# Optimization experiments

Measured on AMD Instinct MI355X. Metric: run time of the kernel, lower is better.

Reference implementation:

```python
import jax, jax.numpy as jnp
import numpy as np

# init config (from init_kwargs)
NUM_ANCHORS = 5
NUM_CLASSES = 80
ANCHORS = jnp.array([[0.57273, 0.677385], [1.87446, 2.06253], [3.33843, 5.47434],
                     [7.88282, 3.52778], [9.77052, 9.16828]], dtype=jnp.float32)
MAX_BOXES = 50  # hard-coded loop bound in build_targets


def setup_inputs() -> dict:
    key = jax.random.key(0)
    k1, k2 = jax.random.split(key)
    output = jax.random.normal(k1, (64, 425, 38, 38), dtype=jnp.float32)
    # target: (nB, 50*5) of [cls, cx, cy, w, h] normalized to (0,1); strictly
    # positive entries -> all 50 boxes valid (original loop breaks at first 0).
    target = jax.random.uniform(k2, (64, 250), dtype=jnp.float32, minval=0.02, maxval=0.98)
    return {"output": output, "target": target, "reqd_class_index": 14}


def _cls_mask(target, nH, nW):
    """Vectorized build_targets: only cls_mask affects the returned loss.
    For each valid GT box, best anchor = argmax IoU of (0,0,aw,ah) vs (0,0,gw,gh)
    (first max wins, matching the strict > in the Python loop); mark cell
    (b, best_n, gj, gi)."""
    nB = target.shape[0]
    tgt = target.reshape(nB, MAX_BOXES, 5)
    # loop breaks at first t with target[b][5t+1]==0 -> cumulative validity
    valid = jnp.cumprod((tgt[:, :, 1] != 0).astype(jnp.int32), axis=1) > 0
    gx = tgt[:, :, 1] * nW
    gy = tgt[:, :, 2] * nH
    gw = tgt[:, :, 3] * nW  # (nB, T)
    gh = tgt[:, :, 4] * nH
    gi = jnp.clip(jnp.floor(gx).astype(jnp.int32), 0, nW - 1)
    gj = jnp.clip(jnp.floor(gy).astype(jnp.int32), 0, nH - 1)
    aw, ah = ANCHORS[:, 0], ANCHORS[:, 1]  # (nA,)
    # centered-box IoU: intersection widths are min of the widths
    inter = jnp.minimum(gw[..., None], aw) * jnp.minimum(gh[..., None], ah)  # (nB,T,nA)
    iou = inter / (gw[..., None] * gh[..., None] + aw * ah - inter)
    best_n = jnp.argmax(iou, axis=-1).astype(jnp.int32)  # (nB, T), first-max tiebreak
    b = jnp.arange(nB, dtype=jnp.int32)[:, None]
    flat = ((b * NUM_ANCHORS + best_n) * nH + gj) * nW + gi  # (nB, T)
    n_cells = nB * NUM_ANCHORS * nH * nW
    mask = jnp.zeros((n_cells,), jnp.int32).at[flat.ravel()].max(valid.ravel().astype(jnp.int32))
    return mask > 0


def reference(output, target, reqd_class_index):
    nB, _, nH, nW = output.shape
    out = output.reshape(nB, NUM_ANCHORS, 5 + NUM_CLASSES, nH, nW)
    # class logits -> (nB, nA, nH, nW, nC), matching torch's
    # view(nB*nA, nC, nH*nW).transpose(1,2).view(-1, nC) flattening order
    cls_logits = jnp.transpose(out[:, :, 5:, :, :], (0, 1, 3, 4, 2))
    probs = jax.nn.softmax(cls_logits, axis=-1)
    p = probs[..., reqd_class_index].reshape(-1)  # prob of required class per cell
    mask = _cls_mask(target, nH, nW)
    m = mask.astype(p.dtype)
    # L1Loss(cls_prob2, 0, size_average=True) over selected cells == masked mean
    loss = jnp.sum(p * m) / jnp.sum(m)
    max_class_prob = jnp.max(jnp.where(mask, p, -jnp.inf))
    return loss, max_class_prob
```

## Files before the change

kernel.cpp:

```cpp
#include <hip/hip_runtime.h>
#include <stdint.h>
#include <math.h>

#define NUM_ANCHORS 5
#define NUM_CLASSES 80
#define MAX_BOXES   50


__global__ void __launch_bounds__(64)
build_list(const float* __restrict__ target,
           int* __restrict__ cnt,
           int* __restrict__ list,
           int nH, int nW) {
#pragma clang fp contract(off)
    int b = blockIdx.x;
    int lane = threadIdx.x;
    const float* t = target + (long)b * MAX_BOXES * 5;
    float x = 1.0f, y = 0.0f, w = 0.0f, h = 0.0f;
    if (lane < MAX_BOXES) {
        x = t[lane * 5 + 1];
        y = t[lane * 5 + 2];
        w = t[lane * 5 + 3];
        h = t[lane * 5 + 4];
    }
    unsigned long long zb = __ballot(lane < MAX_BOXES && x == 0.0f);
    int first_zero = zb ? (__ffsll(zb) - 1) : MAX_BOXES;
    bool valid = lane < first_zero;

    float gx = x * (float)nW;
    float gy = y * (float)nH;
    float gw = w * (float)nW;
    float gh = h * (float)nH;
    int gi = min(max((int)floorf(gx), 0), nW - 1);
    int gj = min(max((int)floorf(gy), 0), nH - 1);

    const float aw[NUM_ANCHORS] = {0.57273f, 1.87446f, 3.33843f, 7.88282f, 9.77052f};
    const float ah[NUM_ANCHORS] = {0.677385f, 2.06253f, 5.47434f, 3.52778f, 9.16828f};
    int best = 0; float bestiou = -1.0f;
    #pragma unroll
    for (int n = 0; n < NUM_ANCHORS; ++n) {
        float inter = fminf(gw, aw[n]) * fminf(gh, ah[n]);
        float uni   = gw * gh + aw[n] * ah[n] - inter;
        float iou   = inter / uni;
        if (iou > bestiou) { bestiou = iou; best = n; }
    }
    int flat = ((b * NUM_ANCHORS + best) * nH + gj) * nW + gi;

    unsigned long long vmask = __ballot(valid);
    bool dup = false;
    for (int j = 0; j < MAX_BOXES; ++j) {
        int fj = __shfl(flat, j, 64);
        dup |= (j < lane) && (((vmask >> j) & 1ull) != 0) && (fj == flat);
    }
    bool keep = valid && !dup;
    unsigned long long kmask = __ballot(keep);
    if (keep) {
        int rank = __popcll(kmask & ((1ull << lane) - 1ull));
        list[b * MAX_BOXES + rank] = flat;
    }
    if (lane == 0) cnt[b] = (int)__popcll(kmask);
}

__global__ void __launch_bounds__(256)
reduce_list(const float* __restrict__ output,
            const int* __restrict__ cnt,
            const int* __restrict__ list,
            float* __restrict__ psum,
            float* __restrict__ pmax,
            const int* __restrict__ reqd,
            int HW, int total) {
    __shared__ float sp[4];
    __shared__ float sm[4];
    int lane = threadIdx.x & 63;
    int wave = threadIdx.x >> 6;
    int g = blockIdx.x * 4 + wave;
    float p = 0.0f, pm = -INFINITY;
    if (g < total) {
        int b    = g / MAX_BOXES;
        int slot = g - b * MAX_BOXES;
        if (slot < cnt[b]) {
            int cell = list[g];
            int ba = cell / HW;
            int hw = cell - ba * HW;
            const float* ptr = output + ((long)(ba * (5 + NUM_CLASSES) + 5)) * HW + hw;
            float v0 = ptr[(long)lane * HW];
            float v1 = (lane < NUM_CLASSES - 64) ? ptr[(long)(lane + 64) * HW] : -INFINITY;
            float mx = fmaxf(v0, v1);
            #pragma unroll
            for (int off = 32; off; off >>= 1) mx = fmaxf(mx, __shfl_xor(mx, off, 64));
            float e0 = expf(v0 - mx);
            float e1 = (lane < NUM_CLASSES - 64) ? expf(v1 - mx) : 0.0f;
            float s = e0 + e1;
            #pragma unroll
            for (int off = 32; off; off >>= 1) s += __shfl_xor(s, off, 64);
            int rq = *reqd;
            float lr = (rq < 64) ? __shfl(v0, rq, 64) : __shfl(v1, rq - 64, 64);
            p = expf(lr - mx) / s;
            pm = p;
        }
    }
    if (lane == 0) { sp[wave] = p; sm[wave] = pm; }
    __syncthreads();
    if (threadIdx.x == 0) {
        float ts = 0.0f, tm = -INFINITY;
        #pragma unroll
        for (int w = 0; w < 4; ++w) { ts += sp[w]; tm = fmaxf(tm, sm[w]); }
        psum[blockIdx.x] = ts;
        pmax[blockIdx.x] = tm;
    }
}

__global__ void __launch_bounds__(1024)
finalize(const int* __restrict__ cnt,
         const float* __restrict__ psum,
         const float* __restrict__ pmax,
         float* __restrict__ out,
         int nblocks, int nB) {
    __shared__ float ss[16];
    __shared__ float sx[16];
    __shared__ int   sc[16];
    int tid = threadIdx.x;
    float s = 0.0f, m = -INFINITY;
    int   c = 0;
    for (int i = tid; i < nblocks; i += 1024) { s += psum[i]; m = fmaxf(m, pmax[i]); }
    if (tid < nB) c = cnt[tid];
    #pragma unroll
    for (int off = 32; off; off >>= 1) {
        s += __shfl_xor(s, off, 64);
        m = fmaxf(m, __shfl_xor(m, off, 64));
        c += __shfl_xor(c, off, 64);
    }
    int lane = tid & 63, wv = tid >> 6;
    if (lane == 0) { ss[wv] = s; sx[wv] = m; sc[wv] = c; }
    __syncthreads();
    if (tid == 0) {
        float S = 0.0f, M = -INFINITY; int C = 0;
        #pragma unroll
        for (int i = 0; i < 16; ++i) { S += ss[i]; M = fmaxf(M, sx[i]); C += sc[i]; }
        out[0] = S / (float)C;
        out[1] = M;
    }
}

extern "C" void kernel_launch(void* const* d_in, const int* in_sizes, int n_in,
                              void* d_out, int out_size, void* d_ws, size_t ws_size,
                              hipStream_t stream) {
    const float* output = (const float*)d_in[0];
    const float* target = (const float*)d_in[1];
    const int*   reqd   = (const int*)d_in[2];
    float* out = (float*)d_out;

    int nB = in_sizes[1] / (MAX_BOXES * 5);
    int HW = in_sizes[0] / (nB * (5 + NUM_CLASSES) * NUM_ANCHORS);
    int nW = 1; while (nW * nW < HW) ++nW;
    int nH = HW / nW;

    int total   = nB * MAX_BOXES;
    int rblocks = (total + 3) / 4;

    uint32_t* ws   = (uint32_t*)d_ws;
    int*      cnt  = (int*)ws;
    int*      list = (int*)(ws + nB);
    float*    psum = (float*)(ws + nB + total);
    float*    pmax = psum + rblocks;

    build_list<<<nB, 64, 0, stream>>>(target, cnt, list, nH, nW);

    reduce_list<<<rblocks, 256, 0, stream>>>(output, cnt, list, psum, pmax,
                                             reqd, HW, total);

    finalize<<<1, 1024, 0, stream>>>(cnt, psum, pmax, out, rblocks, nB);
}
```

Before: 200.8 us.

## Fuse target list building into the gather-reduce kernel

Removes the separate build_list kernel. Each wave now recomputes the per-batch box cells, anchor match and deduplication for its batch, then picks its slot's cell with a ballot rank and an OR-reduction. Per-block counts go to the finalize kernel in place of a per-batch count array. This saves one kernel launch and a global round trip, at the cost of redundant target loads and the 50-iteration shuffle dedup loop running in every wave, 50x per batch.

```diff
diff --git a/kernel.cpp b/kernel.cpp
--- a/kernel.cpp
+++ b/kernel.cpp
@@ -7,79 +7,76 @@
 #define MAX_BOXES   50
 
 
-__global__ void __launch_bounds__(64)
-build_list(const float* __restrict__ target,
-           int* __restrict__ cnt,
-           int* __restrict__ list,
-           int nH, int nW) {
+__global__ void __launch_bounds__(256)
+fused_region_loss(const float* __restrict__ output,
+                  const float* __restrict__ target,
+                  const int* __restrict__ reqd,
+                  float* __restrict__ psum,
+                  float* __restrict__ pmax,
+                  int*   __restrict__ pcnt,
+                  int nH, int nW, int HW, int total) {
 #pragma clang fp contract(off)
-    int b = blockIdx.x;
-    int lane = threadIdx.x;
-    const float* t = target + (long)b * MAX_BOXES * 5;
-    float x = 1.0f, y = 0.0f, w = 0.0f, h = 0.0f;
-    if (lane < MAX_BOXES) {
-        x = t[lane * 5 + 1];
-        y = t[lane * 5 + 2];
-        w = t[lane * 5 + 3];
-        h = t[lane * 5 + 4];
-    }
-    unsigned long long zb = __ballot(lane < MAX_BOXES && x == 0.0f);
-    int first_zero = zb ? (__ffsll(zb) - 1) : MAX_BOXES;
-    bool valid = lane < first_zero;
-
-    float gx = x * (float)nW;
-    float gy = y * (float)nH;
-    float gw = w * (float)nW;
-    float gh = h * (float)nH;
-    int gi = min(max((int)floorf(gx), 0), nW - 1);
-    int gj = min(max((int)floorf(gy), 0), nH - 1);
-
-    const float aw[NUM_ANCHORS] = {0.57273f, 1.87446f, 3.33843f, 7.88282f, 9.77052f};
-    const float ah[NUM_ANCHORS] = {0.677385f, 2.06253f, 5.47434f, 3.52778f, 9.16828f};
-    int best = 0; float bestiou = -1.0f;
-    #pragma unroll
-    for (int n = 0; n < NUM_ANCHORS; ++n) {
-        float inter = fminf(gw, aw[n]) * fminf(gh, ah[n]);
-        float uni   = gw * gh + aw[n] * ah[n] - inter;
-        float iou   = inter / uni;
-        if (iou > bestiou) { bestiou = iou; best = n; }
-    }
-    int flat = ((b * NUM_ANCHORS + best) * nH + gj) * nW + gi;
-
-    unsigned long long vmask = __ballot(valid);
-    bool dup = false;
-    for (int j = 0; j < MAX_BOXES; ++j) {
-        int fj = __shfl(flat, j, 64);
-        dup |= (j < lane) && (((vmask >> j) & 1ull) != 0) && (fj == flat);
-    }
-    bool keep = valid && !dup;
-    unsigned long long kmask = __ballot(keep);
-    if (keep) {
-        int rank = __popcll(kmask & ((1ull << lane) - 1ull));
-        list[b * MAX_BOXES + rank] = flat;
-    }
-    if (lane == 0) cnt[b] = (int)__popcll(kmask);
-}
-
-__global__ void __launch_bounds__(256)
-reduce_list(const float* __restrict__ output,
-            const int* __restrict__ cnt,
-            const int* __restrict__ list,
-            float* __restrict__ psum,
-            float* __restrict__ pmax,
-            const int* __restrict__ reqd,
-            int HW, int total) {
     __shared__ float sp[4];
     __shared__ float sm[4];
+    __shared__ int   sc[4];
     int lane = threadIdx.x & 63;
     int wave = threadIdx.x >> 6;
     int g = blockIdx.x * 4 + wave;
     float p = 0.0f, pm = -INFINITY;
+    int   c = 0;
+
     if (g < total) {
         int b    = g / MAX_BOXES;
         int slot = g - b * MAX_BOXES;
-        if (slot < cnt[b]) {
-            int cell = list[g];
+
+        const float* t = target + (long)b * MAX_BOXES * 5;
+        float x = 1.0f, y = 0.0f, w = 0.0f, h = 0.0f;
+        if (lane < MAX_BOXES) {
+            x = t[lane * 5 + 1];
+            y = t[lane * 5 + 2];
+            w = t[lane * 5 + 3];
+            h = t[lane * 5 + 4];
+        }
+        unsigned long long zb = __ballot(lane < MAX_BOXES && x == 0.0f);
+        int first_zero = zb ? (__ffsll(zb) - 1) : MAX_BOXES;
+        bool valid = lane < first_zero;
+
+        float gx = x * (float)nW;
+        float gy = y * (float)nH;
+        float gw = w * (float)nW;
+        float gh = h * (float)nH;
+        int gi = min(max((int)floorf(gx), 0), nW - 1);
+        int gj = min(max((int)floorf(gy), 0), nH - 1);
+
+        const float aw[NUM_ANCHORS] = {0.57273f, 1.87446f, 3.33843f, 7.88282f, 9.77052f};
+        const float ah[NUM_ANCHORS] = {0.677385f, 2.06253f, 5.47434f, 3.52778f, 9.16828f};
+        int best = 0; float bestiou = -1.0f;
+        #pragma unroll
+        for (int n = 0; n < NUM_ANCHORS; ++n) {
+            float inter = fminf(gw, aw[n]) * fminf(gh, ah[n]);
+            float uni   = gw * gh + aw[n] * ah[n] - inter;
+            float iou   = inter / uni;
+            if (iou > bestiou) { bestiou = iou; best = n; }
+        }
+        int flat = ((b * NUM_ANCHORS + best) * nH + gj) * nW + gi;
+
+        unsigned long long vmask = __ballot(valid);
+        bool dup = false;
+        for (int j = 0; j < MAX_BOXES; ++j) {
+            int fj = __shfl(flat, j, 64);
+            dup |= (j < lane) && (((vmask >> j) & 1ull) != 0) && (fj == flat);
+        }
+        bool keep = valid && !dup;
+        unsigned long long kmask = __ballot(keep);
+        int cnt = (int)__popcll(kmask);
+        if (slot == 0) c = cnt;
+
+        if (slot < cnt) {
+            int rank = keep ? __popcll(kmask & ((1ull << lane) - 1ull)) : -1;
+            int cell = (keep && rank == slot) ? flat : 0;
+            #pragma unroll
+            for (int off = 32; off; off >>= 1) cell |= __shfl_xor(cell, off, 64);
+
             int ba = cell / HW;
             int hw = cell - ba * HW;
             const float* ptr = output + ((long)(ba * (5 + NUM_CLASSES) + 5)) * HW + hw;
@@ -99,31 +96,35 @@
             pm = p;
         }
     }
-    if (lane == 0) { sp[wave] = p; sm[wave] = pm; }
+    if (lane == 0) { sp[wave] = p; sm[wave] = pm; sc[wave] = c; }
     __syncthreads();
     if (threadIdx.x == 0) {
-        float ts = 0.0f, tm = -INFINITY;
+        float ts = 0.0f, tm = -INFINITY; int tc = 0;
         #pragma unroll
-        for (int w = 0; w < 4; ++w) { ts += sp[w]; tm = fmaxf(tm, sm[w]); }
+        for (int w = 0; w < 4; ++w) { ts += sp[w]; tm = fmaxf(tm, sm[w]); tc += sc[w]; }
         psum[blockIdx.x] = ts;
         pmax[blockIdx.x] = tm;
+        pcnt[blockIdx.x] = tc;
     }
 }
 
 __global__ void __launch_bounds__(1024)
-finalize(const int* __restrict__ cnt,
-         const float* __restrict__ psum,
+finalize(const float* __restrict__ psum,
          const float* __restrict__ pmax,
+         const int*   __restrict__ pcnt,
          float* __restrict__ out,
-         int nblocks, int nB) {
+         int nblocks) {
     __shared__ float ss[16];
     __shared__ float sx[16];
     __shared__ int   sc[16];
     int tid = threadIdx.x;
     float s = 0.0f, m = -INFINITY;
     int   c = 0;
-    for (int i = tid; i < nblocks; i += 1024) { s += psum[i]; m = fmaxf(m, pmax[i]); }
-    if (tid < nB) c = cnt[tid];
+    for (int i = tid; i < nblocks; i += 1024) {
+        s += psum[i];
+        m = fmaxf(m, pmax[i]);
+        c += pcnt[i];
+    }
     #pragma unroll
     for (int off = 32; off; off >>= 1) {
         s += __shfl_xor(s, off, 64);
@@ -159,15 +160,13 @@
     int rblocks = (total + 3) / 4;
 
     uint32_t* ws   = (uint32_t*)d_ws;
-    int*      cnt  = (int*)ws;
-    int*      list = (int*)(ws + nB);
-    float*    psum = (float*)(ws + nB + total);
+    float*    psum = (float*)ws;
     float*    pmax = psum + rblocks;
+    int*      pcnt = (int*)(pmax + rblocks);
 
-    build_list<<<nB, 64, 0, stream>>>(target, cnt, list, nH, nW);
+    fused_region_loss<<<rblocks, 256, 0, stream>>>(output, target, reqd,
+                                                   psum, pmax, pcnt,
+                                                   nH, nW, HW, total);
 
-    reduce_list<<<rblocks, 256, 0, stream>>>(output, cnt, list, psum, pmax,
-                                             reqd, HW, total);
-
-    finalize<<<1, 1024, 0, stream>>>(cnt, psum, pmax, out, rblocks, nB);
+    finalize<<<1, 1024, 0, stream>>>(psum, pmax, pcnt, out, rblocks);
 }
```

After: 199.3 us. No clear change (-0.7%).
